# Kernel optimization log

Measured on AMD Instinct MI355X. Metric: run time of the kernel, lower is better.

## Reference

```python
import jax, jax.numpy as jnp
import numpy as np

def setup_inputs() -> dict:
    key = jax.random.key(0)
    k1, k2 = jax.random.split(key)
    pcs1 = jax.random.normal(k1, (8, 4096, 3), dtype=jnp.float32)
    pcs2 = jax.random.normal(k2, (8, 4096, 3), dtype=jnp.float32)
    return {"pcs1": pcs1, "pcs2": pcs2}

def reference(pcs1, pcs2):
    # Pairwise squared L2 distances: [B, N, M]
    # ||a-b||^2 = ||a||^2 + ||b||^2 - 2 a.b
    sq1 = jnp.sum(pcs1 * pcs1, axis=-1)                # [B, N]
    sq2 = jnp.sum(pcs2 * pcs2, axis=-1)                # [B, M]
    inner = jnp.einsum('bnd,bmd->bnm', pcs1, pcs2)     # [B, N, M]
    d = sq1[:, :, None] + sq2[:, None, :] - 2.0 * inner
    d = jnp.maximum(d, 0.0)  # guard tiny negatives from cancellation
    dist1 = jnp.min(d, axis=2)   # [B, N] nearest in pcs2 for each point of pcs1
    dist2 = jnp.min(d, axis=1)   # [B, M] nearest in pcs1 for each point of pcs2
    loss1 = jnp.mean(jnp.sqrt(dist1))
    loss2 = jnp.mean(jnp.sqrt(dist2))
    return (loss1 + loss2) * 0.5
```

## Files before the change

### kernel.cpp

```cpp
#include <hip/hip_runtime.h>
#include <math.h>


typedef __attribute__((ext_vector_type(8)))  short bf16x8;
typedef __attribute__((ext_vector_type(16))) float f32x16;
typedef float f32x2 __attribute__((ext_vector_type(2)));

#define NPTS 4096
#define BATCH 8
#define FRAG_PER_B 8192u

union FragCast { uint4 u; bf16x8 v; };

__device__ __forceinline__ unsigned short f2bf(float f) {
    unsigned u = __float_as_uint(f);
    return (unsigned short)((u + 0x7FFFu + ((u >> 16) & 1u)) >> 16);
}
__device__ __forceinline__ float bf2f(unsigned short h) {
    return __uint_as_float(((unsigned)h) << 16);
}
__device__ __forceinline__ unsigned pk(unsigned short a, unsigned short b) {
    return (unsigned)a | ((unsigned)b << 16);
}

__global__ __launch_bounds__(256) void chamfer_prep(
    const float* __restrict__ pcs1, const float* __restrict__ pcs2,
    uint4* __restrict__ fa1, uint4* __restrict__ fa2,
    uint4* __restrict__ fb1, uint4* __restrict__ fb2,
    float* __restrict__ sqarr)
{
    const int gid   = blockIdx.x * 256 + threadIdx.x;
    const int cloud = gid >> 15;
    const int idx   = gid & 32767;
    const int b     = idx >> 12;
    const int pt    = idx & 4095;

    const float* src = (cloud ? pcs2 : pcs1) + ((size_t)b * NPTS + pt) * 3;
    float x = src[0], y = src[1], z = src[2];
    float sq = fmaf(x, x, fmaf(y, y, z * z));

    float m2x = -2.0f * x, m2y = -2.0f * y, m2z = -2.0f * z;
    unsigned short hx = f2bf(m2x), hy = f2bf(m2y), hz = f2bf(m2z);
    unsigned short lx = f2bf(m2x - bf2f(hx));
    unsigned short ly = f2bf(m2y - bf2f(hy));
    unsigned short lz = f2bf(m2z - bf2f(hz));
    unsigned short sh = f2bf(sq);
    unsigned short sl = f2bf(sq - bf2f(sh));

    unsigned short px = f2bf(x), py = f2bf(y), pz = f2bf(z);
    unsigned short qx = f2bf(x - bf2f(px));
    unsigned short qy = f2bf(y - bf2f(py));
    unsigned short qz = f2bf(z - bf2f(pz));
    const unsigned short ONE = 0x3F80;

    uint4 a0 = make_uint4(pk(hx, hy), pk(hz, hx), pk(hy, hz), pk(lx, ly));
    uint4 a1 = make_uint4(pk(lz, lx), pk(ly, lz), pk(sh, sl), 0u);
    uint4 b0 = make_uint4(pk(px, py), pk(pz, qx), pk(qy, qz), pk(px, py));
    uint4 b1 = make_uint4(pk(pz, qx), pk(qy, qz), pk(ONE, ONE), 0u);

    const int tile = pt >> 5, row = pt & 31;
    const size_t i0 = (size_t)b * FRAG_PER_B + ((size_t)tile * 2 + 0) * 32 + row;
    const size_t i1 = (size_t)b * FRAG_PER_B + ((size_t)tile * 2 + 1) * 32 + row;
    uint4* fa = cloud ? fa2 : fa1;
    uint4* fb = cloud ? fb2 : fb1;
    fa[i0] = a0; fa[i1] = a1;
    fb[i0] = b0; fb[i1] = b1;
    sqarr[((size_t)cloud * 8 + b) * NPTS + pt] = sq;
}

__global__ __launch_bounds__(256, 2) void chamfer_mfma(
    const uint4* __restrict__ fa1, const uint4* __restrict__ fa2,
    const uint4* __restrict__ fb1, const uint4* __restrict__ fb2,
    const float* __restrict__ sqarr, float* __restrict__ partials)
{
    __shared__ uint4 stage[2048];

    const int bid = blockIdx.x;
    const int dir = bid >> 8;
    const int b   = (bid >> 5) & 7;
    const int mch = bid & 31;

    const uint4* fA = (dir ? fa1 : fa2) + (size_t)b * FRAG_PER_B;
    const uint4* fB = (dir ? fb2 : fb1) + (size_t)b * FRAG_PER_B;
    const float* sqB = sqarr + ((size_t)dir * 8 + b) * NPTS;

    const int tid = threadIdx.x;
    const int w   = tid >> 6;
    const int l   = tid & 63;
    const int hf  = l >> 5;
    const int ln  = l & 31;
    const int mtile = mch * 4 + w;

    FragCast bq;
    bq.u = fB[((size_t)mtile * 2 + hf) * 32 + ln];

    const f32x16 cz = {0.f,0.f,0.f,0.f,0.f,0.f,0.f,0.f,
                       0.f,0.f,0.f,0.f,0.f,0.f,0.f,0.f};
    float acc0 = 3.4e38f, acc1 = 3.4e38f;

    for (int phase = 0; phase < 4; ++phase) {
        __syncthreads();
#pragma unroll
        for (int i = 0; i < 8; ++i)
            stage[i * 256 + tid] = fA[(size_t)phase * 2048 + i * 256 + tid];
        __syncthreads();

#pragma unroll 4
        for (int j = 0; j < 32; ++j) {
            FragCast aq;
            aq.u = stage[(j * 2 + hf) * 32 + ln];
            f32x16 D = __builtin_amdgcn_mfma_f32_32x32x16_bf16(
                aq.v, bq.v, cz, 0, 0, 0);
            float m0 = fminf(fminf(D[0],  D[1]),  D[2]);
            float m1 = fminf(fminf(D[3],  D[4]),  D[5]);
            float m2 = fminf(fminf(D[6],  D[7]),  D[8]);
            float m3 = fminf(fminf(D[9],  D[10]), D[11]);
            float m4 = fminf(fminf(D[12], D[13]), D[14]);
            float m5 = fminf(fminf(m0, m1), D[15]);
            float m6 = fminf(fminf(m2, m3), m4);
            if (j & 1) acc1 = fminf(acc1, fminf(m5, m6));
            else       acc0 = fminf(acc0, fminf(m5, m6));
        }
    }

    float accmin = fminf(acc0, acc1);
    accmin = fminf(accmin, __shfl_xor(accmin, 32, 64));

    const int col = mtile * 32 + ln;
    float s = 0.0f;
    if (l < 32) {
        float d = fmaxf(accmin + sqB[col], 0.0f);
        s = sqrtf(d);
    }
#pragma unroll
    for (int off = 1; off < 64; off <<= 1)
        s += __shfl_xor(s, off, 64);
    if (l == 0) partials[bid * 4 + w] = s;
}

__global__ __launch_bounds__(256) void chamfer_final(
    const float* __restrict__ partials, int n, float scale,
    float* __restrict__ out)
{
    __shared__ float ws[4];
    const int t = threadIdx.x;
    float v = 0.0f;
    for (int i = t; i < n; i += 256) v += partials[i];
#pragma unroll
    for (int off = 1; off < 64; off <<= 1) v += __shfl_xor(v, off, 64);
    if ((t & 63) == 0) ws[t >> 6] = v;
    __syncthreads();
    if (t == 0)
        out[0] = (ws[0] + ws[1] + ws[2] + ws[3]) * scale;
}

#define CPAIRS 1024
#define PA 16
#define RSTRIDE 68

__device__ __forceinline__ f32x2 pk_fma_lo(f32x2 c, f32x2 q, f32x2 acc) {
    f32x2 d;
    asm("v_pk_fma_f32 %0, %1, %2, %3 op_sel:[0,0,0] op_sel_hi:[0,1,1]"
        : "=v"(d) : "v"(c), "v"(q), "v"(acc));
    return d;
}
__device__ __forceinline__ f32x2 pk_fma_hi(f32x2 c, f32x2 q, f32x2 acc) {
    f32x2 d;
    asm("v_pk_fma_f32 %0, %1, %2, %3 op_sel:[1,0,0] op_sel_hi:[1,1,1]"
        : "=v"(d) : "v"(c), "v"(q), "v"(acc));
    return d;
}
__device__ __forceinline__ void vmin3(float& acc, float a, float b) {
    asm("v_min3_f32 %0, %1, %2, %3" : "=v"(acc) : "v"(acc), "v"(a), "v"(b));
}

__global__ __launch_bounds__(256, 4) void chamfer_vec(
    const float* __restrict__ pcs1, const float* __restrict__ pcs2,
    float* __restrict__ partials)
{
    __shared__ float4 lds[2 * CPAIRS];
    float4* bx = lds;
    float4* bz = lds + CPAIRS;

    const int bid = blockIdx.x;
    const int dir = bid >> 9;
    const int b   = (bid >> 6) & 7;
    const int ach = bid & 63;

    const float* A  = dir ? pcs2 : pcs1;
    const float* Bp = dir ? pcs1 : pcs2;
    const float* abase = A  + (size_t)b * NPTS * 3;
    const float* bbase = Bp + (size_t)b * NPTS * 3;

    const int tid = threadIdx.x;
    const int w   = tid >> 6;
    const int l   = tid & 63;

    const int apt = ach * 64 + w * PA;
    f32x2 cx[PA / 2], cy[PA / 2], cz2[PA / 2];
    float tmin[PA];
#pragma unroll
    for (int p2 = 0; p2 < PA / 2; ++p2) {
        const float* s = abase + (size_t)(apt + 2 * p2) * 3;
        cx[p2]  = (f32x2){-2.0f * s[0], -2.0f * s[3]};
        cy[p2]  = (f32x2){-2.0f * s[1], -2.0f * s[4]};
        cz2[p2] = (f32x2){-2.0f * s[2], -2.0f * s[5]};
        tmin[2 * p2] = 3.4e38f; tmin[2 * p2 + 1] = 3.4e38f;
    }

    for (int c = 0; c < 2; ++c) {
        if (c) __syncthreads();
#pragma unroll
        for (int i = 0; i < CPAIRS / 256; ++i) {
            int j  = i * 256 + tid;
            const float* s = bbase + (size_t)(c * CPAIRS + j) * 6;
            float x0 = s[0], y0 = s[1], z0 = s[2];
            float x1 = s[3], y1 = s[4], z1 = s[5];
            bx[j] = make_float4(x0, x1, y0, y1);
            bz[j] = make_float4(z0, z1,
                                fmaf(x0, x0, fmaf(y0, y0, z0 * z0)),
                                fmaf(x1, x1, fmaf(y1, y1, z1 * z1)));
        }
        __syncthreads();
#pragma unroll 4
        for (int t = 0; t < CPAIRS / 64; ++t) {
            float4 X = bx[t * 64 + l];
            float4 Z = bz[t * 64 + l];
            f32x2 qx = (f32x2){X.x, X.y};
            f32x2 qy = (f32x2){X.z, X.w};
            f32x2 qz = (f32x2){Z.x, Z.y};
            f32x2 qw = (f32x2){Z.z, Z.w};
#pragma unroll
            for (int p2 = 0; p2 < PA / 2; ++p2) {
                f32x2 d0 = pk_fma_lo(cz2[p2], qz, qw);
                d0 = pk_fma_lo(cy[p2], qy, d0);
                d0 = pk_fma_lo(cx[p2], qx, d0);
                vmin3(tmin[2 * p2], d0.x, d0.y);
                f32x2 d1 = pk_fma_hi(cz2[p2], qz, qw);
                d1 = pk_fma_hi(cy[p2], qy, d1);
                d1 = pk_fma_hi(cx[p2], qx, d1);
                vmin3(tmin[2 * p2 + 1], d1.x, d1.y);
            }
        }
    }

    __syncthreads();
    float* lds2 = (float*)lds;
#pragma unroll
    for (int p = 0; p < PA; ++p)
        lds2[(w * PA + p) * RSTRIDE + l] = tmin[p];
    __syncthreads();

    if (tid < 64) {
        const int g = tid;
        float m = 3.4e38f;
        const float4* row = (const float4*)&lds2[g * RSTRIDE];
#pragma unroll
        for (int i = 0; i < 16; ++i) {
            float4 v = row[i];
            m = fminf(fminf(m, fminf(v.x, v.y)), fminf(v.z, v.w));
        }
        const int ap = ach * 64 + g;
        float x = abase[ap * 3 + 0], y = abase[ap * 3 + 1], z = abase[ap * 3 + 2];
        float s = sqrtf(fmaxf(fmaf(x, x, fmaf(y, y, z * z)) + m, 0.0f));
#pragma unroll
        for (int off = 1; off < 64; off <<= 1) s += __shfl_xor(s, off, 64);
        if (g == 0) partials[bid] = s;
    }
}

extern "C" void kernel_launch(void* const* d_in, const int* in_sizes, int n_in,
                              void* d_out, int out_size, void* d_ws, size_t ws_size,
                              hipStream_t stream) {
    const float* pcs1 = (const float*)d_in[0];
    const float* pcs2 = (const float*)d_in[1];
    float* out = (float*)d_out;

    const size_t MB = 1048576;
    const size_t need = 4 * MB + 256 * 1024 + 8192 + 256;

    if (ws_size >= need) {
        char* w = (char*)d_ws;
        uint4* fa1 = (uint4*)(w + 0 * MB);
        uint4* fa2 = (uint4*)(w + 1 * MB);
        uint4* fb1 = (uint4*)(w + 2 * MB);
        uint4* fb2 = (uint4*)(w + 3 * MB);
        float* sqarr    = (float*)(w + 4 * MB);
        float* partials = (float*)(w + 4 * MB + 256 * 1024);

        chamfer_prep <<<dim3(256), dim3(256), 0, stream>>>(
            pcs1, pcs2, fa1, fa2, fb1, fb2, sqarr);
        chamfer_mfma <<<dim3(512), dim3(256), 0, stream>>>(
            fa1, fa2, fb1, fb2, sqarr, partials);
        chamfer_final<<<dim3(1), dim3(256), 0, stream>>>(
            partials, 2048, 1.0f / 65536.0f, out);
    } else {
        float* partials = (float*)d_ws;
        chamfer_vec  <<<dim3(1024), dim3(256), 0, stream>>>(pcs1, pcs2, partials);
        chamfer_final<<<dim3(1),    dim3(256), 0, stream>>>(
            partials, 1024, 1.0f / 65536.0f, out);
    }
}
```

Before: 25.42 us.

## Split MFMA distance kernel over A halves with atomicMin and fold squared norm into MFMA

Each work block now covers only half of the A points, doubling the grid to 1024 blocks with higher occupancy bounds. Per-column minima are merged across halves with atomicMin on float bits into a dist buffer that the prep kernel initialises to +inf. The B squared norm is folded into the MFMA through an extra fragment slot, which removes the sqarr load. Two reduction kernels replace the single final one. This adds a kernel launch and atomic traffic in exchange for better use of the CUs.

```diff
diff --git a/kernel.cpp b/kernel.cpp
--- a/kernel.cpp
+++ b/kernel.cpp
@@ -27,13 +27,15 @@
     const float* __restrict__ pcs1, const float* __restrict__ pcs2,
     uint4* __restrict__ fa1, uint4* __restrict__ fa2,
     uint4* __restrict__ fb1, uint4* __restrict__ fb2,
-    float* __restrict__ sqarr)
+    unsigned* __restrict__ dist)
 {
     const int gid   = blockIdx.x * 256 + threadIdx.x;
     const int cloud = gid >> 15;
     const int idx   = gid & 32767;
     const int b     = idx >> 12;
     const int pt    = idx & 4095;
+
+    dist[gid] = 0x7F800000u;
 
     const float* src = (cloud ? pcs2 : pcs1) + ((size_t)b * NPTS + pt) * 3;
     float x = src[0], y = src[1], z = src[2];
@@ -54,9 +56,9 @@
     const unsigned short ONE = 0x3F80;
 
     uint4 a0 = make_uint4(pk(hx, hy), pk(hz, hx), pk(hy, hz), pk(lx, ly));
-    uint4 a1 = make_uint4(pk(lz, lx), pk(ly, lz), pk(sh, sl), 0u);
+    uint4 a1 = make_uint4(pk(lz, lx), pk(ly, lz), pk(sh, sl), pk(ONE, ONE));
     uint4 b0 = make_uint4(pk(px, py), pk(pz, qx), pk(qy, qz), pk(px, py));
-    uint4 b1 = make_uint4(pk(pz, qx), pk(qy, qz), pk(ONE, ONE), 0u);
+    uint4 b1 = make_uint4(pk(pz, qx), pk(qy, qz), pk(ONE, ONE), pk(sh, sl));
 
     const int tile = pt >> 5, row = pt & 31;
     const size_t i0 = (size_t)b * FRAG_PER_B + ((size_t)tile * 2 + 0) * 32 + row;
@@ -65,24 +67,24 @@
     uint4* fb = cloud ? fb2 : fb1;
     fa[i0] = a0; fa[i1] = a1;
     fb[i0] = b0; fb[i1] = b1;
-    sqarr[((size_t)cloud * 8 + b) * NPTS + pt] = sq;
-}
-
-__global__ __launch_bounds__(256, 2) void chamfer_mfma(
+}
+
+__global__ __launch_bounds__(256, 4) void chamfer_mfma(
     const uint4* __restrict__ fa1, const uint4* __restrict__ fa2,
     const uint4* __restrict__ fb1, const uint4* __restrict__ fb2,
-    const float* __restrict__ sqarr, float* __restrict__ partials)
+    unsigned* __restrict__ dist)
 {
     __shared__ uint4 stage[2048];
 
-    const int bid = blockIdx.x;
-    const int dir = bid >> 8;
-    const int b   = (bid >> 5) & 7;
-    const int mch = bid & 31;
-
-    const uint4* fA = (dir ? fa1 : fa2) + (size_t)b * FRAG_PER_B;
+    const int bid  = blockIdx.x;
+    const int dir  = bid >> 9;
+    const int b    = (bid >> 6) & 7;
+    const int mch  = (bid >> 1) & 31;
+    const int half = bid & 1;
+
+    const uint4* fA = (dir ? fa1 : fa2) + (size_t)b * FRAG_PER_B
+                      + (size_t)half * 4096;
     const uint4* fB = (dir ? fb2 : fb1) + (size_t)b * FRAG_PER_B;
-    const float* sqB = sqarr + ((size_t)dir * 8 + b) * NPTS;
 
     const int tid = threadIdx.x;
     const int w   = tid >> 6;
@@ -98,60 +100,66 @@
                        0.f,0.f,0.f,0.f,0.f,0.f,0.f,0.f};
     float acc0 = 3.4e38f, acc1 = 3.4e38f;
 
-    for (int phase = 0; phase < 4; ++phase) {
+    for (int phase = 0; phase < 2; ++phase) {
         __syncthreads();
 #pragma unroll
         for (int i = 0; i < 8; ++i)
             stage[i * 256 + tid] = fA[(size_t)phase * 2048 + i * 256 + tid];
         __syncthreads();
 
-#pragma unroll 4
-        for (int j = 0; j < 32; ++j) {
-            FragCast aq;
-            aq.u = stage[(j * 2 + hf) * 32 + ln];
-            f32x16 D = __builtin_amdgcn_mfma_f32_32x32x16_bf16(
-                aq.v, bq.v, cz, 0, 0, 0);
-            float m0 = fminf(fminf(D[0],  D[1]),  D[2]);
-            float m1 = fminf(fminf(D[3],  D[4]),  D[5]);
-            float m2 = fminf(fminf(D[6],  D[7]),  D[8]);
-            float m3 = fminf(fminf(D[9],  D[10]), D[11]);
-            float m4 = fminf(fminf(D[12], D[13]), D[14]);
-            float m5 = fminf(fminf(m0, m1), D[15]);
-            float m6 = fminf(fminf(m2, m3), m4);
-            if (j & 1) acc1 = fminf(acc1, fminf(m5, m6));
-            else       acc0 = fminf(acc0, fminf(m5, m6));
+#pragma unroll 2
+        for (int j2 = 0; j2 < 16; ++j2) {
+            FragCast aq0, aq1;
+            aq0.u = stage[(j2 * 4 + 0 + hf) * 32 + ln];
+            aq1.u = stage[(j2 * 4 + 2 + hf) * 32 + ln];
+            f32x16 D0 = __builtin_amdgcn_mfma_f32_32x32x16_bf16(
+                aq0.v, bq.v, cz, 0, 0, 0);
+            f32x16 D1 = __builtin_amdgcn_mfma_f32_32x32x16_bf16(
+                aq1.v, bq.v, cz, 0, 0, 0);
+#pragma unroll
+            for (int i = 0; i < 8; ++i)
+                acc0 = fminf(fminf(acc0, D0[2 * i]), D0[2 * i + 1]);
+#pragma unroll
+            for (int i = 0; i < 8; ++i)
+                acc1 = fminf(fminf(acc1, D1[2 * i]), D1[2 * i + 1]);
         }
     }
 
     float accmin = fminf(acc0, acc1);
     accmin = fminf(accmin, __shfl_xor(accmin, 32, 64));
 
-    const int col = mtile * 32 + ln;
-    float s = 0.0f;
     if (l < 32) {
-        float d = fmaxf(accmin + sqB[col], 0.0f);
-        s = sqrtf(d);
-    }
-#pragma unroll
-    for (int off = 1; off < 64; off <<= 1)
-        s += __shfl_xor(s, off, 64);
-    if (l == 0) partials[bid * 4 + w] = s;
-}
-
-__global__ __launch_bounds__(256) void chamfer_final(
-    const float* __restrict__ partials, int n, float scale,
-    float* __restrict__ out)
+        const int col = mtile * 32 + ln;
+        float d = fmaxf(accmin, 0.0f);
+        atomicMin(&dist[(((unsigned)dir * 8 + b) << 12) + col],
+                  __float_as_uint(d));
+    }
+}
+
+__global__ __launch_bounds__(256) void chamfer_red1(
+    const unsigned* __restrict__ dist, float* __restrict__ bpart)
 {
     __shared__ float ws[4];
     const int t = threadIdx.x;
-    float v = 0.0f;
-    for (int i = t; i < n; i += 256) v += partials[i];
-#pragma unroll
-    for (int off = 1; off < 64; off <<= 1) v += __shfl_xor(v, off, 64);
-    if ((t & 63) == 0) ws[t >> 6] = v;
+    const uint4* d4 = (const uint4*)dist;
+    uint4 v = d4[blockIdx.x * 256 + t];
+    float s = sqrtf(__uint_as_float(v.x)) + sqrtf(__uint_as_float(v.y))
+            + sqrtf(__uint_as_float(v.z)) + sqrtf(__uint_as_float(v.w));
+#pragma unroll
+    for (int off = 1; off < 64; off <<= 1) s += __shfl_xor(s, off, 64);
+    if ((t & 63) == 0) ws[t >> 6] = s;
     __syncthreads();
     if (t == 0)
-        out[0] = (ws[0] + ws[1] + ws[2] + ws[3]) * scale;
+        bpart[blockIdx.x] = ws[0] + ws[1] + ws[2] + ws[3];
+}
+
+__global__ __launch_bounds__(64) void chamfer_red2(
+    const float* __restrict__ bpart, float* __restrict__ out)
+{
+    float v = bpart[threadIdx.x];
+#pragma unroll
+    for (int off = 1; off < 64; off <<= 1) v += __shfl_xor(v, off, 64);
+    if (threadIdx.x == 0) out[0] = v * (1.0f / 65536.0f);
 }
 
 #define CPAIRS 1024
@@ -269,6 +277,22 @@
     }
 }
 
+__global__ __launch_bounds__(256) void chamfer_final(
+    const float* __restrict__ partials, int n, float scale,
+    float* __restrict__ out)
+{
+    __shared__ float ws[4];
+    const int t = threadIdx.x;
+    float v = 0.0f;
+    for (int i = t; i < n; i += 256) v += partials[i];
+#pragma unroll
+    for (int off = 1; off < 64; off <<= 1) v += __shfl_xor(v, off, 64);
+    if ((t & 63) == 0) ws[t >> 6] = v;
+    __syncthreads();
+    if (t == 0)
+        out[0] = (ws[0] + ws[1] + ws[2] + ws[3]) * scale;
+}
+
 extern "C" void kernel_launch(void* const* d_in, const int* in_sizes, int n_in,
                               void* d_out, int out_size, void* d_ws, size_t ws_size,
                               hipStream_t stream) {
@@ -277,7 +301,7 @@
     float* out = (float*)d_out;
 
     const size_t MB = 1048576;
-    const size_t need = 4 * MB + 256 * 1024 + 8192 + 256;
+    const size_t need = 4 * MB + 256 * 1024 + 1024;
 
     if (ws_size >= need) {
         char* w = (char*)d_ws;
@@ -285,15 +309,15 @@
         uint4* fa2 = (uint4*)(w + 1 * MB);
         uint4* fb1 = (uint4*)(w + 2 * MB);
         uint4* fb2 = (uint4*)(w + 3 * MB);
-        float* sqarr    = (float*)(w + 4 * MB);
-        float* partials = (float*)(w + 4 * MB + 256 * 1024);
-
-        chamfer_prep <<<dim3(256), dim3(256), 0, stream>>>(
-            pcs1, pcs2, fa1, fa2, fb1, fb2, sqarr);
-        chamfer_mfma <<<dim3(512), dim3(256), 0, stream>>>(
-            fa1, fa2, fb1, fb2, sqarr, partials);
-        chamfer_final<<<dim3(1), dim3(256), 0, stream>>>(
-            partials, 2048, 1.0f / 65536.0f, out);
+        unsigned* dist = (unsigned*)(w + 4 * MB);
+        float* bpart   = (float*)(w + 4 * MB + 256 * 1024);
+
+        chamfer_prep<<<dim3(256),  dim3(256), 0, stream>>>(
+            pcs1, pcs2, fa1, fa2, fb1, fb2, dist);
+        chamfer_mfma<<<dim3(1024), dim3(256), 0, stream>>>(
+            fa1, fa2, fb1, fb2, dist);
+        chamfer_red1<<<dim3(64),   dim3(256), 0, stream>>>(dist, bpart);
+        chamfer_red2<<<dim3(1),    dim3(64),  0, stream>>>(bpart, out);
     } else {
         float* partials = (float*)d_ws;
         chamfer_vec  <<<dim3(1024), dim3(256), 0, stream>>>(pcs1, pcs2, partials);
```

New measurement: 23.02 us. 9.4% less time.
